# Optimization experiments

Hardware: AMD Instinct MI355X
Metric: run time of the kernel (lower is better)

Reference implementation:

```python
import jax, jax.numpy as jnp
import numpy as np


def setup_inputs() -> dict:
    key = jax.random.key(0)
    kx, kh, kwx, kwh = jax.random.split(key, 4)
    N, T, D, H = 32, 1024, 512, 512
    x = jax.random.normal(kx, (N, T, D), dtype=jnp.float32)
    h0 = jax.random.normal(kh, (N, H), dtype=jnp.float32)
    Wx = jax.random.normal(kwx, (D, 4 * H), dtype=jnp.float32) / jnp.sqrt(jnp.float32(D))
    Wh = jax.random.normal(kwh, (H, 4 * H), dtype=jnp.float32) / jnp.sqrt(jnp.float32(H))
    b = jnp.zeros((4 * H,), dtype=jnp.float32)
    return {"x": x, "h0": h0, "Wx": Wx, "Wh": Wh, "b": b}


def _lstm_forward(x, h0, Wx, Wh, b):
    N, T, D = x.shape
    H = h0.shape[1]
    # Precompute input-to-hidden projection for all timesteps as one GEMM.
    xW = jnp.einsum("ntd,df->ntf", x, Wx) + b  # (N, T, 4H)

    def step(carry, xw_t):
        prev_h, prev_c = carry
        a = xw_t + prev_h @ Wh  # (N, 4H)
        a_i, a_f, a_o, a_g = jnp.split(a, 4, axis=-1)  # gate order: i, f, o, g
        i = jax.nn.sigmoid(a_i)
        f = jax.nn.sigmoid(a_f)
        o = jax.nn.sigmoid(a_o)
        g = jnp.tanh(a_g)
        next_c = f * prev_c + i * g
        next_h = o * jnp.tanh(next_c)
        return (next_h, next_c), next_h

    c0 = jnp.zeros_like(h0)
    xW_t = jnp.swapaxes(xW, 0, 1)  # (T, N, 4H) for scan over time
    _, hs = jax.lax.scan(step, (h0, c0), xW_t)
    return jnp.swapaxes(hs, 0, 1)  # (N, T, H)


def reference(x, h0, Wx, Wh, b):
    return _lstm_forward(x, h0, Wx, Wh, b)
```

## Files before the change

### kernel.cpp

```cpp
#include <hip/hip_runtime.h>
#include <hip/hip_bf16.h>

typedef __bf16 bf16x8 __attribute__((ext_vector_type(8)));
typedef float  f32x4  __attribute__((ext_vector_type(4)));
typedef float  f32x8  __attribute__((ext_vector_type(8)));
typedef int    i32x4  __attribute__((ext_vector_type(4)));

#define T_LEN 1024
#define DD    512
#define HH    512
#define NBLK  64
#define DEPTH 8
#define FSTRIDE 8

__device__ __forceinline__ f32x4 mfma16(bf16x8 a, bf16x8 b, f32x4 c) {
    return __builtin_amdgcn_mfma_f32_16x16x32_bf16(a, b, c, 0, 0, 0);
}
__device__ __forceinline__ float sigmf_(float v) { return 1.f / (1.f + __expf(-v)); }
__device__ __forceinline__ float tanhf_(float v) { return 1.f - 2.f / (1.f + __expf(2.f * v)); }
__device__ __forceinline__ bf16x8 cvt8(f32x8 v) {
    bf16x8 r;
    #pragma unroll
    for (int j = 0; j < 8; ++j) r[j] = (__bf16)v[j];
    return r;
}

__device__ __forceinline__ void poll17(const unsigned short* p, const float* rp,
                                       i32x4 f[16], i32x4* rv) {
    for (;;) {
        asm volatile(
            "global_load_dwordx4 %16, %18, off sc1\n\t"
            "global_load_dwordx4 %0, %17, off sc1\n\t"
            "global_load_dwordx4 %1, %17, off offset:64 sc1\n\t"
            "global_load_dwordx4 %2, %17, off offset:128 sc1\n\t"
            "global_load_dwordx4 %3, %17, off offset:192 sc1\n\t"
            "global_load_dwordx4 %4, %17, off offset:256 sc1\n\t"
            "global_load_dwordx4 %5, %17, off offset:320 sc1\n\t"
            "global_load_dwordx4 %6, %17, off offset:384 sc1\n\t"
            "global_load_dwordx4 %7, %17, off offset:448 sc1\n\t"
            "global_load_dwordx4 %8, %17, off offset:512 sc1\n\t"
            "global_load_dwordx4 %9, %17, off offset:576 sc1\n\t"
            "global_load_dwordx4 %10, %17, off offset:640 sc1\n\t"
            "global_load_dwordx4 %11, %17, off offset:704 sc1\n\t"
            "global_load_dwordx4 %12, %17, off offset:768 sc1\n\t"
            "global_load_dwordx4 %13, %17, off offset:832 sc1\n\t"
            "global_load_dwordx4 %14, %17, off offset:896 sc1\n\t"
            "global_load_dwordx4 %15, %17, off offset:960 sc1\n\t"
            "s_waitcnt vmcnt(0)"
            : "=&v"(f[0]), "=&v"(f[1]), "=&v"(f[2]), "=&v"(f[3]),
              "=&v"(f[4]), "=&v"(f[5]), "=&v"(f[6]), "=&v"(f[7]),
              "=&v"(f[8]), "=&v"(f[9]), "=&v"(f[10]), "=&v"(f[11]),
              "=&v"(f[12]), "=&v"(f[13]), "=&v"(f[14]), "=&v"(f[15]),
              "=&v"(*rv)
            : "v"(p), "v"(rp)
            : "memory");
        unsigned mn = 0xffffffffu;
        #pragma unroll
        for (int kk = 0; kk < 16; ++kk) {
            mn = min(mn, (unsigned)f[kk][0] & 0xffffu);
            mn = min(mn, (unsigned)f[kk][2] & 0xffffu);
        }
        int ok = (mn != 0u) & ((*rv)[0] != 0) & ((*rv)[2] != 0);
        if (__all(ok)) break;
        __builtin_amdgcn_s_sleep(1);
    }
}

__device__ __forceinline__ i32x4 poll_ring(const float* rp) {
    i32x4 rv;
    for (;;) {
        asm volatile(
            "global_load_dwordx4 %0, %1, off sc1\n\t"
            "s_waitcnt vmcnt(0)"
            : "=&v"(rv) : "v"(rp) : "memory");
        if (__all((rv[0] != 0) & (rv[2] != 0))) break;
        __builtin_amdgcn_s_sleep(1);
    }
    return rv;
}

__device__ __forceinline__ void xpart_mfma(const float* xr, const bf16x8* wbh, const bf16x8* wbl,
                                           f32x4& ac0, f32x4& ac1, f32x4& ac2, f32x4& ac3) {
    #pragma unroll
    for (int kk = 0; kk < 16; ++kk) {
        bf16x8 av = cvt8(*(const f32x8*)(xr + kk * 32));
        if (kk & 1) { ac1 = mfma16(av, wbh[kk], ac1); ac3 = mfma16(av, wbl[kk], ac3); }
        else        { ac0 = mfma16(av, wbh[kk], ac0); ac2 = mfma16(av, wbl[kk], ac2); }
    }
}

__global__ void __launch_bounds__(256, 1)
lstm_pk(const float* __restrict__ x,
        const float* __restrict__ h0,
        const float* __restrict__ Wx,
        const float* __restrict__ Wh,
        const float* __restrict__ bias,
        float* __restrict__ out,
        unsigned short* __restrict__ ws16,
        unsigned* __restrict__ progress,
        float* __restrict__ ring)
{
    __shared__ float a_lds[32][36];

    const int tid  = threadIdx.x;
    const bool isprod = (blockIdx.x >= NBLK);
    const int blk  = isprod ? (blockIdx.x - NBLK) : blockIdx.x;
    const int hc0  = blk * 8;
    const int lane = tid & 63;
    const int wid  = tid >> 6;
    const int q    = lane >> 4;
    const int mrow = (wid & 1) * 16 + (lane & 15);
    const int bcol = (wid >> 1) * 16 + (lane & 15);
    const int gcol = (bcol >> 3) * HH + hc0 + (bcol & 7);

    const float* wsrc = isprod ? Wx : Wh;
    bf16x8 wbh[16], wbl[16];
    #pragma unroll
    for (int kk = 0; kk < 16; ++kk) {
        const int kb = kk * 32 + q * 8;
        bf16x8 wh_, wl_;
        #pragma unroll
        for (int j = 0; j < 8; ++j) {
            float w = wsrc[(size_t)(kb + j) * (4 * HH) + gcol];
            __bf16 hi = (__bf16)w;
            wh_[j] = hi;
            wl_[j] = (__bf16)(w - (float)hi);
        }
        wbh[kk] = wh_; wbl[kk] = wl_;
    }

    float* rbase = ring + (size_t)blk * DEPTH * 1024;

    if (isprod) {
        const float* xrow0 = x + (size_t)mrow * T_LEN * DD + q * 8;
        unsigned last = 0;
        #pragma unroll 1
        for (int t = 0; t < T_LEN; ++t) {
            while (t >= (int)last + DEPTH) {
                last = __hip_atomic_load(progress + blk * FSTRIDE,
                                         __ATOMIC_RELAXED, __HIP_MEMORY_SCOPE_AGENT);
                if (t >= (int)last + DEPTH) __builtin_amdgcn_s_sleep(8);
            }
            f32x4 a0 = {0,0,0,0}, a1 = {0,0,0,0}, a2 = {0,0,0,0}, a3 = {0,0,0,0};
            xpart_mfma(xrow0 + (size_t)t * DD, wbh, wbl, a0, a1, a2, a3);
            f32x4 s = (a0 + a1) + (a2 + a3);
            unsigned u0 = __float_as_uint(s[0]); if (!u0) u0 = 1u;
            unsigned u1 = __float_as_uint(s[1]); if (!u1) u1 = 1u;
            unsigned u2 = __float_as_uint(s[2]); if (!u2) u2 = 1u;
            unsigned u3 = __float_as_uint(s[3]); if (!u3) u3 = 1u;
            unsigned long long lo = ((unsigned long long)u1 << 32) | u0;
            unsigned long long hi = ((unsigned long long)u3 << 32) | u2;
            unsigned long long* dst =
                (unsigned long long*)(rbase + (size_t)(t & (DEPTH - 1)) * 1024 + tid * 4);
            __hip_atomic_store(dst,     lo, __ATOMIC_RELAXED, __HIP_MEMORY_SCOPE_AGENT);
            __hip_atomic_store(dst + 1, hi, __ATOMIC_RELAXED, __HIP_MEMORY_SCOPE_AGENT);
        }
        return;
    }

    const int gn  = tid >> 3;
    const int glc = tid & 7;
    const float bi  = bias[0 * HH + hc0 + glc];
    const float bf_ = bias[1 * HH + hc0 + glc];
    const float bo  = bias[2 * HH + hc0 + glc];
    const float bg  = bias[3 * HH + hc0 + glc];
    float creg = 0.f;
    const size_t outoff = (size_t)gn * T_LEN * HH + hc0 + glc;

    unsigned short* u16out = (unsigned short*)out;
    const unsigned short* cbase =
        (const unsigned short*)out + 2 * ((size_t)mrow * T_LEN * HH) + q * 8;
    const size_t stash_w = 2 * ((size_t)gn * T_LEN * HH) + (hc0 + glc);
    const unsigned short* wsrd = ws16 + (size_t)mrow * HH + q * 8;
    const size_t ws_w = (size_t)gn * HH + (hc0 + glc);

    #pragma unroll 1
    for (int t = 0; t < T_LEN; ++t) {
        const float* rp = rbase + (size_t)(t & (DEPTH - 1)) * 1024 + tid * 4;
        bf16x8 hfrag[16];
        i32x4 rv;
        if (t == 0) {
            #pragma unroll
            for (int kk = 0; kk < 16; ++kk)
                hfrag[kk] = cvt8(*(const f32x8*)(h0 + (size_t)mrow * HH + kk * 32 + q * 8));
            rv = poll_ring(rp);
        } else {
            i32x4 f[16];
            if (t < T_LEN - 1)
                poll17(cbase + 2 * (size_t)(t + 1) * HH, rp, f, &rv);
            else
                poll17(wsrd, rp, f, &rv);
            #pragma unroll
            for (int kk = 0; kk < 16; ++kk) hfrag[kk] = *(bf16x8*)&f[kk];
        }

        f32x4 ac0 = {0,0,0,0}, ac1 = {0,0,0,0}, ac2 = {0,0,0,0}, ac3 = {0,0,0,0};
        #pragma unroll
        for (int kk = 0; kk < 16; ++kk) {
            if (kk & 1) { ac1 = mfma16(hfrag[kk], wbh[kk], ac1); ac3 = mfma16(hfrag[kk], wbl[kk], ac3); }
            else        { ac0 = mfma16(hfrag[kk], wbh[kk], ac0); ac2 = mfma16(hfrag[kk], wbl[kk], ac2); }
        }
        f32x4 av4 = (ac0 + ac1) + (ac2 + ac3);
        av4[0] += __uint_as_float(rv[0]);
        av4[1] += __uint_as_float(rv[1]);
        av4[2] += __uint_as_float(rv[2]);
        av4[3] += __uint_as_float(rv[3]);

        {
            unsigned long long* zp = (unsigned long long*)rp;
            __hip_atomic_store(zp,     0ull, __ATOMIC_RELAXED, __HIP_MEMORY_SCOPE_AGENT);
            __hip_atomic_store(zp + 1, 0ull, __ATOMIC_RELAXED, __HIP_MEMORY_SCOPE_AGENT);
        }

        __syncthreads();
        if (tid == 0)
            __hip_atomic_store(progress + blk * FSTRIDE, (unsigned)t,
                               __ATOMIC_RELAXED, __HIP_MEMORY_SCOPE_AGENT);
        #pragma unroll
        for (int r = 0; r < 4; ++r)
            a_lds[(wid & 1) * 16 + q * 4 + r][bcol] = av4[r];
        __syncthreads();

        float ai = a_lds[gn][glc]      + bi;
        float af = a_lds[gn][8 + glc]  + bf_;
        float ao = a_lds[gn][16 + glc] + bo;
        float ag = a_lds[gn][24 + glc] + bg;
        float iv = sigmf_(ai), fv = sigmf_(af), ov = sigmf_(ao);
        float gv = tanhf_(ag);
        creg = fv * creg + iv * gv;
        float hv = ov * tanhf_(creg);

        unsigned hvu = __float_as_uint(hv);
        unsigned long long opair =
            ((unsigned long long)__shfl_xor(hvu, 1) << 32) | (unsigned long long)hvu;
        __bf16 hb = (__bf16)hv;
        unsigned short hus = *(unsigned short*)&hb;
        if (hus == 0) hus = 1;
        unsigned hu = (unsigned)hus;
        unsigned hp = (__shfl_xor(hu, 1) << 16) | hu;
        unsigned long long hq =
            ((unsigned long long)__shfl_xor(hp, 2) << 32) | (unsigned long long)hp;

        if ((glc & 1) == 0)
            __hip_atomic_store((unsigned long long*)(out + outoff + (size_t)t * HH),
                               opair, __ATOMIC_RELAXED, __HIP_MEMORY_SCOPE_AGENT);
        if ((glc & 3) == 0) {
            if (t < T_LEN - 2)
                __hip_atomic_store((unsigned long long*)(u16out + stash_w + 2 * (size_t)(t + 2) * HH),
                                   hq, __ATOMIC_RELAXED, __HIP_MEMORY_SCOPE_AGENT);
            else if (t == T_LEN - 2)
                __hip_atomic_store((unsigned long long*)(ws16 + ws_w),
                                   hq, __ATOMIC_RELAXED, __HIP_MEMORY_SCOPE_AGENT);
        }
    }
}

extern "C" void kernel_launch(void* const* d_in, const int* in_sizes, int n_in,
                              void* d_out, int out_size, void* d_ws, size_t ws_size,
                              hipStream_t stream) {
    const float* x  = (const float*)d_in[0];
    const float* h0 = (const float*)d_in[1];
    const float* Wx = (const float*)d_in[2];
    const float* Wh = (const float*)d_in[3];
    const float* b  = (const float*)d_in[4];
    float* out = (float*)d_out;
    unsigned short* ws16 = (unsigned short*)d_ws;
    unsigned* progress   = (unsigned*)((char*)d_ws + 32768);
    float* ring          = (float*)((char*)d_ws + 65536);
    const size_t ring_bytes = (size_t)NBLK * DEPTH * 1024 * sizeof(float);

    hipMemsetAsync(out, 0, (size_t)32 * T_LEN * HH * sizeof(float), stream);
    hipMemsetAsync(d_ws, 0, 65536 + ring_bytes, stream);
    lstm_pk<<<dim3(2 * NBLK), dim3(256), 0, stream>>>(x, h0, Wx, Wh, b, out,
                                                      ws16, progress, ring);
}
```

Before: 5.249 ms.

## Exchange hidden state via epoch-tagged small ring instead of output stash

```diff
diff --git a/kernel.cpp b/kernel.cpp
--- a/kernel.cpp
+++ b/kernel.cpp
@@ -11,6 +11,7 @@
 #define HH    512
 #define NBLK  64
 #define DEPTH 8
+#define HSLOTS 4
 #define FSTRIDE 8
 
 __device__ __forceinline__ f32x4 mfma16(bf16x8 a, bf16x8 b, f32x4 c) {
@@ -25,45 +26,40 @@
     return r;
 }
 
-__device__ __forceinline__ void poll17(const unsigned short* p, const float* rp,
-                                       i32x4 f[16], i32x4* rv) {
-    for (;;) {
-        asm volatile(
-            "global_load_dwordx4 %16, %18, off sc1\n\t"
-            "global_load_dwordx4 %0, %17, off sc1\n\t"
-            "global_load_dwordx4 %1, %17, off offset:64 sc1\n\t"
-            "global_load_dwordx4 %2, %17, off offset:128 sc1\n\t"
-            "global_load_dwordx4 %3, %17, off offset:192 sc1\n\t"
-            "global_load_dwordx4 %4, %17, off offset:256 sc1\n\t"
-            "global_load_dwordx4 %5, %17, off offset:320 sc1\n\t"
-            "global_load_dwordx4 %6, %17, off offset:384 sc1\n\t"
-            "global_load_dwordx4 %7, %17, off offset:448 sc1\n\t"
-            "global_load_dwordx4 %8, %17, off offset:512 sc1\n\t"
-            "global_load_dwordx4 %9, %17, off offset:576 sc1\n\t"
-            "global_load_dwordx4 %10, %17, off offset:640 sc1\n\t"
-            "global_load_dwordx4 %11, %17, off offset:704 sc1\n\t"
-            "global_load_dwordx4 %12, %17, off offset:768 sc1\n\t"
-            "global_load_dwordx4 %13, %17, off offset:832 sc1\n\t"
-            "global_load_dwordx4 %14, %17, off offset:896 sc1\n\t"
-            "global_load_dwordx4 %15, %17, off offset:960 sc1\n\t"
-            "s_waitcnt vmcnt(0)"
-            : "=&v"(f[0]), "=&v"(f[1]), "=&v"(f[2]), "=&v"(f[3]),
-              "=&v"(f[4]), "=&v"(f[5]), "=&v"(f[6]), "=&v"(f[7]),
-              "=&v"(f[8]), "=&v"(f[9]), "=&v"(f[10]), "=&v"(f[11]),
-              "=&v"(f[12]), "=&v"(f[13]), "=&v"(f[14]), "=&v"(f[15]),
-              "=&v"(*rv)
-            : "v"(p), "v"(rp)
-            : "memory");
-        unsigned mn = 0xffffffffu;
-        #pragma unroll
-        for (int kk = 0; kk < 16; ++kk) {
-            mn = min(mn, (unsigned)f[kk][0] & 0xffffu);
-            mn = min(mn, (unsigned)f[kk][2] & 0xffffu);
-        }
-        int ok = (mn != 0u) & ((*rv)[0] != 0) & ((*rv)[2] != 0);
-        if (__all(ok)) break;
-        __builtin_amdgcn_s_sleep(1);
-    }
+__device__ __forceinline__ void issue16(const unsigned* b, i32x4 f[16]) {
+    asm volatile(
+        "global_load_dwordx4 %0, %16, off sc1\n\t"
+        "global_load_dwordx4 %1, %16, off offset:128 sc1\n\t"
+        "global_load_dwordx4 %2, %16, off offset:256 sc1\n\t"
+        "global_load_dwordx4 %3, %16, off offset:384 sc1\n\t"
+        "global_load_dwordx4 %4, %16, off offset:512 sc1\n\t"
+        "global_load_dwordx4 %5, %16, off offset:640 sc1\n\t"
+        "global_load_dwordx4 %6, %16, off offset:768 sc1\n\t"
+        "global_load_dwordx4 %7, %16, off offset:896 sc1\n\t"
+        "global_load_dwordx4 %8, %16, off offset:1024 sc1\n\t"
+        "global_load_dwordx4 %9, %16, off offset:1152 sc1\n\t"
+        "global_load_dwordx4 %10, %16, off offset:1280 sc1\n\t"
+        "global_load_dwordx4 %11, %16, off offset:1408 sc1\n\t"
+        "global_load_dwordx4 %12, %16, off offset:1536 sc1\n\t"
+        "global_load_dwordx4 %13, %16, off offset:1664 sc1\n\t"
+        "global_load_dwordx4 %14, %16, off offset:1792 sc1\n\t"
+        "global_load_dwordx4 %15, %16, off offset:1920 sc1"
+        : "=&v"(f[0]), "=&v"(f[1]), "=&v"(f[2]), "=&v"(f[3]),
+          "=&v"(f[4]), "=&v"(f[5]), "=&v"(f[6]), "=&v"(f[7]),
+          "=&v"(f[8]), "=&v"(f[9]), "=&v"(f[10]), "=&v"(f[11]),
+          "=&v"(f[12]), "=&v"(f[13]), "=&v"(f[14]), "=&v"(f[15])
+        : "v"(b)
+        : "memory");
+}
+
+__device__ __forceinline__ void issue1(const float* p, i32x4* rv) {
+    asm volatile("global_load_dwordx4 %0, %1, off sc1"
+                 : "=&v"(*rv) : "v"(p) : "memory");
+}
+
+__device__ __forceinline__ void wait_all() {
+    asm volatile("s_waitcnt vmcnt(0)" ::: "memory");
+    __builtin_amdgcn_sched_barrier(0);
 }
 
 __device__ __forceinline__ i32x4 poll_ring(const float* rp) {
@@ -79,6 +75,15 @@
     return rv;
 }
 
+__device__ __forceinline__ bf16x8 unpack_hi(i32x4 a, i32x4 b) {
+    i32x4 r;
+    r[0] = (int)(((unsigned)a[1] & 0xFFFF0000u) | ((unsigned)a[0] >> 16));
+    r[1] = (int)(((unsigned)a[3] & 0xFFFF0000u) | ((unsigned)a[2] >> 16));
+    r[2] = (int)(((unsigned)b[1] & 0xFFFF0000u) | ((unsigned)b[0] >> 16));
+    r[3] = (int)(((unsigned)b[3] & 0xFFFF0000u) | ((unsigned)b[2] >> 16));
+    return *(bf16x8*)&r;
+}
+
 __device__ __forceinline__ void xpart_mfma(const float* xr, const bf16x8* wbh, const bf16x8* wbl,
                                            f32x4& ac0, f32x4& ac1, f32x4& ac2, f32x4& ac3) {
     #pragma unroll
@@ -96,7 +101,7 @@
         const float* __restrict__ Wh,
         const float* __restrict__ bias,
         float* __restrict__ out,
-        unsigned short* __restrict__ ws16,
+        unsigned* __restrict__ hring,
         unsigned* __restrict__ progress,
         float* __restrict__ ring)
 {
@@ -167,12 +172,8 @@
     float creg = 0.f;
     const size_t outoff = (size_t)gn * T_LEN * HH + hc0 + glc;
 
-    unsigned short* u16out = (unsigned short*)out;
-    const unsigned short* cbase =
-        (const unsigned short*)out + 2 * ((size_t)mrow * T_LEN * HH) + q * 8;
-    const size_t stash_w = 2 * ((size_t)gn * T_LEN * HH) + (hc0 + glc);
-    const unsigned short* wsrd = ws16 + (size_t)mrow * HH + q * 8;
-    const size_t ws_w = (size_t)gn * HH + (hc0 + glc);
+    const unsigned* hrd = hring + (size_t)mrow * HH + q * 8;
+    unsigned* hwr = hring + (size_t)gn * HH + hc0 + glc;
 
     #pragma unroll 1
     for (int t = 0; t < T_LEN; ++t) {
@@ -185,13 +186,29 @@
                 hfrag[kk] = cvt8(*(const f32x8*)(h0 + (size_t)mrow * HH + kk * 32 + q * 8));
             rv = poll_ring(rp);
         } else {
-            i32x4 f[16];
-            if (t < T_LEN - 1)
-                poll17(cbase + 2 * (size_t)(t + 1) * HH, rp, f, &rv);
-            else
-                poll17(wsrd, rp, f, &rv);
+            const unsigned* ha = hrd + (size_t)((t - 1) & (HSLOTS - 1)) * 16384;
+            const unsigned* hb = ha + 4;
+            const unsigned ep = (unsigned)t;
+            i32x4 fa[16], fb[16];
+            for (;;) {
+                issue16(ha, fa);
+                issue16(hb, fb);
+                issue1(rp, &rv);
+                wait_all();
+                unsigned ok = 1u;
+                #pragma unroll
+                for (int kk = 0; kk < 16; ++kk) {
+                    ok &= ((unsigned)fa[kk][0] & 0xFFFFu) == ep;
+                    ok &= ((unsigned)fa[kk][2] & 0xFFFFu) == ep;
+                    ok &= ((unsigned)fb[kk][0] & 0xFFFFu) == ep;
+                    ok &= ((unsigned)fb[kk][2] & 0xFFFFu) == ep;
+                }
+                ok &= (unsigned)((rv[0] != 0) & (rv[2] != 0));
+                if (__all((int)ok)) break;
+                __builtin_amdgcn_s_sleep(1);
+            }
             #pragma unroll
-            for (int kk = 0; kk < 16; ++kk) hfrag[kk] = *(bf16x8*)&f[kk];
+            for (int kk = 0; kk < 16; ++kk) hfrag[kk] = unpack_hi(fa[kk], fb[kk]);
         }
 
         f32x4 ac0 = {0,0,0,0}, ac1 = {0,0,0,0}, ac2 = {0,0,0,0}, ac3 = {0,0,0,0};
@@ -233,24 +250,17 @@
         unsigned hvu = __float_as_uint(hv);
         unsigned long long opair =
             ((unsigned long long)__shfl_xor(hvu, 1) << 32) | (unsigned long long)hvu;
-        __bf16 hb = (__bf16)hv;
-        unsigned short hus = *(unsigned short*)&hb;
-        if (hus == 0) hus = 1;
-        unsigned hu = (unsigned)hus;
-        unsigned hp = (__shfl_xor(hu, 1) << 16) | hu;
-        unsigned long long hq =
-            ((unsigned long long)__shfl_xor(hp, 2) << 32) | (unsigned long long)hp;
-
-        if ((glc & 1) == 0)
+        __bf16 hb16 = (__bf16)hv;
+        unsigned hw32 = ((unsigned)*(unsigned short*)&hb16 << 16) | ((unsigned)(t + 1) & 0xFFFFu);
+        unsigned long long hpair =
+            ((unsigned long long)__shfl_xor(hw32, 1) << 32) | (unsigned long long)hw32;
+
+        if ((glc & 1) == 0) {
             __hip_atomic_store((unsigned long long*)(out + outoff + (size_t)t * HH),
                                opair, __ATOMIC_RELAXED, __HIP_MEMORY_SCOPE_AGENT);
-        if ((glc & 3) == 0) {
-            if (t < T_LEN - 2)
-                __hip_atomic_store((unsigned long long*)(u16out + stash_w + 2 * (size_t)(t + 2) * HH),
-                                   hq, __ATOMIC_RELAXED, __HIP_MEMORY_SCOPE_AGENT);
-            else if (t == T_LEN - 2)
-                __hip_atomic_store((unsigned long long*)(ws16 + ws_w),
-                                   hq, __ATOMIC_RELAXED, __HIP_MEMORY_SCOPE_AGENT);
+            if (t < T_LEN - 1)
+                __hip_atomic_store((unsigned long long*)(hwr + (size_t)(t & (HSLOTS - 1)) * 16384),
+                                   hpair, __ATOMIC_RELAXED, __HIP_MEMORY_SCOPE_AGENT);
         }
     }
 }
@@ -264,13 +274,13 @@
     const float* Wh = (const float*)d_in[3];
     const float* b  = (const float*)d_in[4];
     float* out = (float*)d_out;
-    unsigned short* ws16 = (unsigned short*)d_ws;
-    unsigned* progress   = (unsigned*)((char*)d_ws + 32768);
-    float* ring          = (float*)((char*)d_ws + 65536);
-    const size_t ring_bytes = (size_t)NBLK * DEPTH * 1024 * sizeof(float);
-
-    hipMemsetAsync(out, 0, (size_t)32 * T_LEN * HH * sizeof(float), stream);
-    hipMemsetAsync(d_ws, 0, 65536 + ring_bytes, stream);
+    unsigned* progress = (unsigned*)d_ws;
+    unsigned* hring    = (unsigned*)((char*)d_ws + 4096);
+    float* ring        = (float*)((char*)d_ws + 4096 + (size_t)HSLOTS * 32 * HH * 4);
+    const size_t init_bytes = 4096 + (size_t)HSLOTS * 32 * HH * 4
+                            + (size_t)NBLK * DEPTH * 1024 * sizeof(float);
+
+    hipMemsetAsync(d_ws, 0, init_bytes, stream);
     lstm_pk<<<dim3(2 * NBLK), dim3(256), 0, stream>>>(x, h0, Wx, Wh, b, out,
-                                                      ws16, progress, ring);
-}
+                                                      hring, progress, ring);
+}
```

New measurement: 9.964 ms. 1.9x slower.
